# Optimization experiments

Measured on AMD Instinct MI355X. Metric: run time of the kernel, lower is better.

The kernel has to match this reference:

```python
import jax, jax.numpy as jnp
import numpy as np

M, N, F = 512, 128, 512  # molecules, atoms per molecule, feature dim
HID, OUT = F // 4, 1


def setup_inputs() -> dict:
    key = jax.random.key(0)
    k1, k2, k3 = jax.random.split(key, 3)
    h = jax.random.normal(k1, (M, N, F), dtype=jnp.float32)
    W1 = jax.random.normal(k2, (F, HID), dtype=jnp.float32) * (1.0 / np.sqrt(F))
    b1 = jnp.zeros((HID,), dtype=jnp.float32)
    W2 = jax.random.normal(k3, (HID, OUT), dtype=jnp.float32) * (1.0 / np.sqrt(HID))
    b2 = jnp.zeros((OUT,), dtype=jnp.float32)
    return {"h": h, "W1": W1, "b1": b1, "W2": W2, "b2": b2}


def reference(h, W1, b1, W2, b2):
    # method == 'weighted_summation'
    # gate MLP: Linear -> ReLU -> Linear -> Sigmoid, per atom
    w = jax.nn.sigmoid(jax.nn.relu(h @ W1 + b1) @ W2 + b2)  # [M, N, OUT]
    # per-molecule weighted sum over atoms: mm(w_h.T, h) for each molecule,
    # concatenated along dim 0 -> [M*OUT, F] (OUT=1 -> [M, F])
    out = jnp.einsum('mno,mnf->mof', w, h)  # [M, OUT, F]
    return out.reshape(M * OUT, F)
```

## Files before the change

### kernel.cpp

```cpp
#include <hip/hip_runtime.h>
#include <hip/hip_bf16.h>


typedef unsigned short u16;
typedef unsigned int u32;
typedef __bf16 bf16x8 __attribute__((ext_vector_type(8)));
typedef float f32x4 __attribute__((ext_vector_type(4)));
typedef u32 u32x4 __attribute__((ext_vector_type(4)));

#define M_MOL 512
#define N_ATOM 128
#define F_DIM 512
#define HID_DIM 128

static __device__ __forceinline__ u16 f2bf(float x) {
  u32 u = __float_as_uint(x);
  u32 r = (u + 0x7fffu + ((u >> 16) & 1u)) >> 16;
  return (u16)r;
}
static __device__ __forceinline__ bf16x8 pack8(u32x4 a, u32x4 b) {
  u32x4 r;
  r[0] = (a[0] >> 16) | (a[1] & 0xffff0000u);
  r[1] = (a[2] >> 16) | (a[3] & 0xffff0000u);
  r[2] = (b[0] >> 16) | (b[1] & 0xffff0000u);
  r[3] = (b[2] >> 16) | (b[3] & 0xffff0000u);
  return __builtin_bit_cast(bf16x8, r);
}

__global__ __launch_bounds__(256) void transpose_w1(const float* __restrict__ W1,
                                                    u16* __restrict__ W1Tt) {
  __shared__ float tile[64][65];
  const int k0 = blockIdx.x * 64;
  const int n0 = blockIdx.y * 64;
  const int t = threadIdx.x;
  #pragma unroll
  for (int i = 0; i < 16; ++i) {
    const int lin = i * 256 + t;
    const int lr = lin >> 6, lc = lin & 63;
    tile[lc][lr] = W1[(size_t)(k0 + lr) * HID_DIM + (n0 + lc)];
  }
  __syncthreads();
  #pragma unroll
  for (int i = 0; i < 16; ++i) {
    const int lin = i * 256 + t;
    const int wr = lin >> 6, wc = lin & 63;
    const int k = k0 + wc;
    W1Tt[(size_t)(k >> 5) * (HID_DIM * 32) + (size_t)(n0 + wr) * 32 + (k & 31)] =
        f2bf(tile[wr][wc]);
  }
}

__global__ __launch_bounds__(512, 2) void pool_mol(
    const float* __restrict__ h, const u16* __restrict__ W1Tt,
    const float* __restrict__ b1, const float* __restrict__ W2,
    const float* __restrict__ b2, float* __restrict__ out) {
  __shared__ u16 As[N_ATOM * F_DIM];
  __shared__ float red[8][F_DIM];
  __shared__ float w_s[N_ATOM];

  const int m = blockIdx.x;
  const int tid = threadIdx.x;
  const int wv = tid >> 6;
  const int lane = tid & 63;
  const int quad = lane >> 4;
  const int cl = lane & 15;

  const int row = wv * 16 + cl;
  const float* hr = h + ((size_t)m * N_ATOM + row) * F_DIM;
  const u32x4* ap = (const u32x4*)hr + quad * 2;
  u32x4 a32[16][2];
  #pragma unroll
  for (int ks = 0; ks < 16; ++ks) {
    a32[ks][0] = ap[ks * 8];
    a32[ks][1] = ap[ks * 8 + 1];
  }

  const u16* bg = W1Tt + cl * 32 + quad * 8;
  u32x4 bf[3][8];
  #pragma unroll
  for (int p = 0; p < 2; ++p)
    #pragma unroll
    for (int t = 0; t < 8; ++t)
      bf[p][t] = *(const u32x4*)(bg + (size_t)p * (HID_DIM * 32) + t * 512);

  bf16x8 ah[16];
  #pragma unroll
  for (int ks = 0; ks < 16; ++ks) {
    ah[ks] = pack8(a32[ks][0], a32[ks][1]);
    const int c = ks * 4 + quad;
    const int phys = (c & ~7) | ((c ^ cl) & 7);
    *(bf16x8*)(As + row * F_DIM + phys * 8) = ah[ks];
  }

  f32x4 acc[8];
  #pragma unroll
  for (int t = 0; t < 8; ++t) acc[t] = (f32x4){0.f, 0.f, 0.f, 0.f};

  #pragma unroll
  for (int ks = 0; ks < 16; ++ks) {
    if (ks < 14) {
      #pragma unroll
      for (int t = 0; t < 8; ++t)
        bf[(ks + 2) % 3][t] =
            *(const u32x4*)(bg + (size_t)(ks + 2) * (HID_DIM * 32) + t * 512);
    }
    #pragma unroll
    for (int t = 0; t < 8; ++t)
      acc[t] = __builtin_amdgcn_mfma_f32_16x16x32_bf16(
          ah[ks], __builtin_bit_cast(bf16x8, bf[ks % 3][t]), acc[t], 0, 0, 0);
  }

  float psum[4] = {0.f, 0.f, 0.f, 0.f};
  #pragma unroll
  for (int t = 0; t < 8; ++t) {
    const int hid = t * 16 + cl;
    const float b1v = b1[hid];
    const float w2v = W2[hid];
    #pragma unroll
    for (int r = 0; r < 4; ++r) {
      float tv = fmaxf(acc[t][r] + b1v, 0.f);
      psum[r] = fmaf(tv, w2v, psum[r]);
    }
  }
  #pragma unroll
  for (int off = 1; off < 16; off <<= 1)
    #pragma unroll
    for (int r = 0; r < 4; ++r)
      psum[r] += __shfl_xor(psum[r], off, 64);
  if (cl == 0) {
    const float b2v = b2[0];
    #pragma unroll
    for (int r = 0; r < 4; ++r)
      w_s[wv * 16 + quad * 4 + r] = 1.f / (1.f + __expf(-(psum[r] + b2v)));
  }
  asm volatile("s_waitcnt lgkmcnt(0)" ::: "memory");
  __builtin_amdgcn_sched_barrier(0);

  float facc[8] = {0.f, 0.f, 0.f, 0.f, 0.f, 0.f, 0.f, 0.f};
  #pragma unroll 4
  for (int i = 0; i < 16; ++i) {
    const int r = wv * 16 + i;
    const float wn = w_s[r];
    const int phys = (lane & ~7) | ((lane ^ i) & 7);
    bf16x8 hv = *(const bf16x8*)(As + r * F_DIM + phys * 8);
    u32x4 uv = __builtin_bit_cast(u32x4, hv);
    #pragma unroll
    for (int j = 0; j < 4; ++j) {
      facc[2 * j]     = fmaf(wn, __uint_as_float(uv[j] << 16), facc[2 * j]);
      facc[2 * j + 1] = fmaf(wn, __uint_as_float(uv[j] & 0xffff0000u), facc[2 * j + 1]);
    }
  }

  #pragma unroll
  for (int j = 0; j < 8; ++j) red[wv][lane * 8 + j] = facc[j];
  __syncthreads();

  {
    const int f = tid;
    float o = 0.f;
    #pragma unroll
    for (int w = 0; w < 8; ++w) o += red[w][f];
    out[(size_t)m * F_DIM + f] = o;
  }
}

extern "C" void kernel_launch(void* const* d_in, const int* in_sizes, int n_in,
                              void* d_out, int out_size, void* d_ws, size_t ws_size,
                              hipStream_t stream) {
  const float* h  = (const float*)d_in[0];
  const float* W1 = (const float*)d_in[1];
  const float* b1 = (const float*)d_in[2];
  const float* W2 = (const float*)d_in[3];
  const float* b2 = (const float*)d_in[4];
  float* out = (float*)d_out;

  u16* W1Tt = (u16*)d_ws;

  transpose_w1<<<dim3(8, 2), 256, 0, stream>>>(W1, W1Tt);
  pool_mol<<<M_MOL, 512, 0, stream>>>(h, W1Tt, b1, W2, b2, out);
}
```

Before: 207.1 us.

## Split each molecule across two 64-atom blocks with a separate reduction kernel

Each molecule's atoms are now handled by two 256-thread blocks of 64 atoms instead of one 512-thread block of 128 atoms. This halves shared memory per block (64KB instead of 128KB+) so more blocks can be resident per CU and the grid doubles. Partial weighted sums go to a workspace buffer, and a new reduce kernel adds the two partials per molecule. The cost is an extra kernel launch plus extra global traffic for the partials.

```diff
diff --git a/kernel.cpp b/kernel.cpp
--- a/kernel.cpp
+++ b/kernel.cpp
@@ -6,12 +6,15 @@
 typedef unsigned int u32;
 typedef __bf16 bf16x8 __attribute__((ext_vector_type(8)));
 typedef float f32x4 __attribute__((ext_vector_type(4)));
+typedef float f32x2 __attribute__((ext_vector_type(2)));
 typedef u32 u32x4 __attribute__((ext_vector_type(4)));
 
 #define M_MOL 512
 #define N_ATOM 128
 #define F_DIM 512
 #define HID_DIM 128
+#define ABLK 64
+#define NBLK (M_MOL * 2)
 
 static __device__ __forceinline__ u16 f2bf(float x) {
   u32 u = __float_as_uint(x);
@@ -50,23 +53,23 @@
   }
 }
 
-__global__ __launch_bounds__(512, 2) void pool_mol(
+__global__ __launch_bounds__(256, 2) void pool_part(
     const float* __restrict__ h, const u16* __restrict__ W1Tt,
     const float* __restrict__ b1, const float* __restrict__ W2,
-    const float* __restrict__ b2, float* __restrict__ out) {
-  __shared__ u16 As[N_ATOM * F_DIM];
-  __shared__ float red[8][F_DIM];
-  __shared__ float w_s[N_ATOM];
+    const float* __restrict__ b2, float* __restrict__ part) {
+  __shared__ u16 As[ABLK * F_DIM];
+  __shared__ float red[4][F_DIM];
+  __shared__ float w_s[ABLK];
 
-  const int m = blockIdx.x;
+  const int blk = blockIdx.x;
   const int tid = threadIdx.x;
   const int wv = tid >> 6;
   const int lane = tid & 63;
   const int quad = lane >> 4;
   const int cl = lane & 15;
 
-  const int row = wv * 16 + cl;
-  const float* hr = h + ((size_t)m * N_ATOM + row) * F_DIM;
+  const int lrow = wv * 16 + cl;
+  const float* hr = h + ((size_t)blk * ABLK + lrow) * F_DIM;
   const u32x4* ap = (const u32x4*)hr + quad * 2;
   u32x4 a32[16][2];
   #pragma unroll
@@ -89,7 +92,7 @@
     ah[ks] = pack8(a32[ks][0], a32[ks][1]);
     const int c = ks * 4 + quad;
     const int phys = (c & ~7) | ((c ^ cl) & 7);
-    *(bf16x8*)(As + row * F_DIM + phys * 8) = ah[ks];
+    *(bf16x8*)(As + lrow * F_DIM + phys * 8) = ah[ks];
   }
 
   f32x4 acc[8];
@@ -156,12 +159,24 @@
   __syncthreads();
 
   {
-    const int f = tid;
-    float o = 0.f;
-    #pragma unroll
-    for (int w = 0; w < 8; ++w) o += red[w][f];
-    out[(size_t)m * F_DIM + f] = o;
+    const int f = tid * 2;
+    f32x2 o;
+    o[0] = red[0][f] + red[1][f] + red[2][f] + red[3][f];
+    o[1] = red[0][f + 1] + red[1][f + 1] + red[2][f + 1] + red[3][f + 1];
+    *(f32x2*)(part + (size_t)blk * F_DIM + f) = o;
   }
+}
+
+__global__ __launch_bounds__(256) void reduce_out(const float* __restrict__ part,
+                                                  float* __restrict__ out) {
+  const int m = blockIdx.x;
+  const int f = threadIdx.x * 2;
+  f32x2 a = *(const f32x2*)(part + (size_t)(2 * m) * F_DIM + f);
+  f32x2 b = *(const f32x2*)(part + (size_t)(2 * m + 1) * F_DIM + f);
+  f32x2 o;
+  o[0] = a[0] + b[0];
+  o[1] = a[1] + b[1];
+  *(f32x2*)(out + (size_t)m * F_DIM + f) = o;
 }
 
 extern "C" void kernel_launch(void* const* d_in, const int* in_sizes, int n_in,
@@ -175,7 +190,9 @@
   float* out = (float*)d_out;
 
   u16* W1Tt = (u16*)d_ws;
+  float* part = (float*)((char*)d_ws + (size_t)HID_DIM * F_DIM * sizeof(u16));
 
   transpose_w1<<<dim3(8, 2), 256, 0, stream>>>(W1, W1Tt);
-  pool_mol<<<M_MOL, 512, 0, stream>>>(h, W1Tt, b1, W2, b2, out);
+  pool_part<<<NBLK, 256, 0, stream>>>(h, W1Tt, b1, W2, b2, part);
+  reduce_out<<<M_MOL, 256, 0, stream>>>(part, out);
 }
```

Measured after the change: 212.0 us. +2.4%, slower.
